# Optimization experiments

Hardware: AMD Instinct MI355X
Metric: run time of the kernel (lower is better)

## Reference

```python
import jax, jax.numpy as jnp
import numpy as np
import math

D_MODEL = 1024
N_HEADS = 16
D_HEAD = D_MODEL // N_HEADS
WINDOW = 256
SCALE = 1.0 / math.sqrt(D_HEAD)


def setup_inputs() -> dict:
    key = jax.random.key(0)
    kx, kqkv, kout = jax.random.split(key, 3)
    x = jax.random.normal(kx, (2, 2048, D_MODEL), dtype=jnp.float32)
    # xavier_uniform for nn.Linear weights (shape [out, in] in torch; store as [in, out] for x @ W)
    lim_qkv = math.sqrt(6.0 / (D_MODEL + 3 * D_MODEL))
    W_qkv = jax.random.uniform(kqkv, (D_MODEL, 3 * D_MODEL), dtype=jnp.float32, minval=-lim_qkv, maxval=lim_qkv)
    lim_out = math.sqrt(6.0 / (D_MODEL + D_MODEL))
    W_out = jax.random.uniform(kout, (D_MODEL, D_MODEL), dtype=jnp.float32, minval=-lim_out, maxval=lim_out)
    return {"x": x, "W_qkv": W_qkv, "W_out": W_out}


def _window_mask(seq_len: int) -> jnp.ndarray:
    # causal + sliding window: position i attends to j with i-WINDOW < j <= i
    i = jnp.arange(seq_len)[:, None]
    j = jnp.arange(seq_len)[None, :]
    allowed = (j <= i) & (j > i - WINDOW)
    return jnp.where(allowed, 0.0, -jnp.inf).astype(jnp.float32)


def reference(x, W_qkv, W_out):
    B, S, _ = x.shape
    qkv = x @ W_qkv                                   # [B, S, 3*D]
    qkv = qkv.reshape(B, S, 3, N_HEADS, D_HEAD)
    qkv = jnp.transpose(qkv, (2, 0, 3, 1, 4))         # [3, B, H, S, Dh]
    q, k, v = qkv[0], qkv[1], qkv[2]
    scores = jnp.einsum('bhsd,bhtd->bhst', q, k) * SCALE
    scores = scores + _window_mask(S)[None, None]
    weights = jax.nn.softmax(scores, axis=-1)
    out = jnp.einsum('bhst,bhtd->bhsd', weights, v)   # [B, H, S, Dh]
    out = jnp.transpose(out, (0, 2, 1, 3)).reshape(B, S, D_MODEL)
    return out @ W_out
```

## Files before the change

### kernel.cpp

```cpp
#include <hip/hip_runtime.h>

typedef unsigned short u16;
typedef unsigned int u32;

#define D_MODEL 1024
#define N_HEADS 16
#define D_HEAD 64
#define WIN 256
#define SEQ 2048
#define BATCH 2
#define NROWS (BATCH*SEQ)

typedef short frag_ab __attribute__((ext_vector_type(8)));
typedef float frag_cd __attribute__((ext_vector_type(4)));
typedef float f32x16 __attribute__((ext_vector_type(16)));
typedef u16 u16x8 __attribute__((ext_vector_type(8)));

__device__ __forceinline__ u16 f2bf(float f) {
    union { float f; u32 u; } x; x.f = f;
    u32 r = x.u + 0x7fffu + ((x.u >> 16) & 1u);
    return (u16)(r >> 16);
}

__device__ __forceinline__ void load_lds16(const void* g, void* l) {
    __builtin_amdgcn_global_load_lds(
        (const __attribute__((address_space(1))) void*)g,
        (__attribute__((address_space(3))) void*)l, 16, 0, 0);
}

__device__ __forceinline__ void transpose_tile(const float* __restrict__ W, u16* __restrict__ WT,
                                               int K, int N, int n0, int k0,
                                               int scale_rows, float scale, float (*tile)[33]) {
    int x = threadIdx.x & 31, y = threadIdx.x >> 5;
#pragma unroll
    for (int r = 0; r < 4; r++)
        tile[y + 8 * r][x] = W[(size_t)(k0 + y + 8 * r) * N + n0 + x];
    __syncthreads();
#pragma unroll
    for (int r = 0; r < 4; r++) {
        int nrow = n0 + y + 8 * r;
        float v = tile[x][y + 8 * r];
        if (nrow < scale_rows) v *= scale;
        WT[(size_t)nrow * K + k0 + x] = f2bf(v);
    }
}

__global__ __launch_bounds__(256) void prep_kernel(const float* __restrict__ x,
                                                   const float* __restrict__ W_qkv,
                                                   u16* __restrict__ xb,
                                                   u16* __restrict__ wqkvT,
                                                   float qscale) {
    __shared__ float tile[32][33];
    const int bid = blockIdx.x;
    if (bid < 4096) {
        int idx = bid * 256 + threadIdx.x;
        float4 v = ((const float4*)x)[idx];
        ushort4 o;
        o.x = f2bf(v.x); o.y = f2bf(v.y); o.z = f2bf(v.z); o.w = f2bf(v.w);
        ((ushort4*)xb)[idx] = o;
    } else {
        int t = bid - 4096;
        transpose_tile(W_qkv, wqkvT, D_MODEL, 3 * D_MODEL, (t % 96) * 32, (t / 96) * 32,
                       D_MODEL, qscale, tile);
    }
}

template <bool BF16_OUT, int BM, int MB, int NPER>
__global__ __launch_bounds__(256, 4) void gemm_bk64(const u16* __restrict__ A,
                                                    const u16* __restrict__ BT,
                                                    void* __restrict__ C,
                                                    int M, int N, int K) {
    constexpr int MT = BM / 64;
    __shared__ union SMem {
        struct { u16 As[BM * 64]; u16 Bs[128 * 64]; } s;
        u16 cs[BF16_OUT ? BM * 136 : 1];
    } sm;
    const int tid = threadIdx.x;
    const int xcd = blockIdx.x & 7, sblk = blockIdx.x >> 3;
    const int m0 = (sblk % MB) * BM;
    const int n0 = (xcd * NPER + sblk / MB) * 128;
    const int wave = tid >> 6, lane = tid & 63;
    const int wm = (wave >> 1) * (BM / 2), wn = (wave & 1) * 64;
    const int l32 = lane & 31, kh = lane >> 5;

    f32x16 acc[MT][2] = {};

    const int r0 = tid >> 3;
    const int w  = (tid & 7) ^ (r0 & 7);
    const u16* aP = A  + (size_t)(m0 + r0) * K + w * 8;
    const u16* bP = BT + (size_t)(n0 + r0) * K + w * 8;

    for (int k0 = 0; k0 < K; k0 += 64) {
        __syncthreads();
#pragma unroll
        for (int u = 0; u < BM / 32; u++)
            load_lds16(aP + (size_t)(32 * u) * K + k0, &sm.s.As[(tid + 256 * u) * 8]);
#pragma unroll
        for (int u = 0; u < 4; u++)
            load_lds16(bP + (size_t)(32 * u) * K + k0, &sm.s.Bs[(tid + 256 * u) * 8]);
        __syncthreads();

#pragma unroll
        for (int kk = 0; kk < 4; kk++) {
            const int csel = ((kk * 2 + kh) ^ (l32 & 7)) * 8;
            frag_ab af[MT], bf[2];
#pragma unroll
            for (int t = 0; t < MT; t++)
                af[t] = *(const frag_ab*)&sm.s.As[(wm + t * 32 + l32) * 64 + csel];
#pragma unroll
            for (int t = 0; t < 2; t++)
                bf[t] = *(const frag_ab*)&sm.s.Bs[(wn + t * 32 + l32) * 64 + csel];
#pragma unroll
            for (int mt = 0; mt < MT; mt++)
#pragma unroll
                for (int nt = 0; nt < 2; nt++)
                    acc[mt][nt] = __builtin_amdgcn_mfma_f32_32x32x16_bf16(af[mt], bf[nt], acc[mt][nt], 0, 0, 0);
        }
    }

    if constexpr (BF16_OUT) {
        __syncthreads();
#pragma unroll
        for (int mt = 0; mt < MT; mt++)
#pragma unroll
            for (int nt = 0; nt < 2; nt++) {
                int col = wn + nt * 32 + l32;
#pragma unroll
                for (int reg = 0; reg < 16; reg++) {
                    int row = wm + mt * 32 + (reg & 3) + 8 * (reg >> 2) + 4 * kh;
                    sm.cs[row * 136 + col] = f2bf(acc[mt][nt][reg]);
                }
            }
        __syncthreads();
        const int cc = tid & 15, rb = tid >> 4;
#pragma unroll
        for (int i = 0; i < BM / 16; i++) {
            int row = rb + 16 * i;
            u16x8 vv = *(const u16x8*)&sm.cs[row * 136 + cc * 8];
            *(u16x8*)((u16*)C + (size_t)(m0 + row) * N + n0 + cc * 8) = vv;
        }
    } else {
#pragma unroll
        for (int mt = 0; mt < MT; mt++)
#pragma unroll
            for (int nt = 0; nt < 2; nt++) {
                int col = n0 + wn + nt * 32 + l32;
#pragma unroll
                for (int reg = 0; reg < 16; reg++) {
                    int row = m0 + wm + mt * 32 + (reg & 3) + 8 * (reg >> 2) + 4 * kh;
                    ((float*)C)[(size_t)row * N + col] = acc[mt][nt][reg];
                }
            }
    }
}

__global__ __launch_bounds__(256) void attn_kernel(const u16* __restrict__ qkv, u16* __restrict__ out,
                                                   const float* __restrict__ W_out,
                                                   u16* __restrict__ woutT) {
    __shared__ u16 Ks[2][64 * 64];
    __shared__ u16 Vt[64 * 72];
    __shared__ u16 ps[4][16 * 72];

    if (blockIdx.x >= 1024) {
        int t = blockIdx.x - 1024;
        transpose_tile(W_out, woutT, D_MODEL, D_MODEL, (t & 31) * 32, (t >> 5) * 32,
                       0, 1.0f, (float(*)[33])&Ks[0][0]);
        return;
    }

    const int tid = threadIdx.x;
    const int wave = tid >> 6, lane = tid & 63;
    const int quad = lane >> 4, c16 = lane & 15;

    const int bh = blockIdx.x & 31;
    const int qc = blockIdx.x >> 5;
    const int h  = bh & 15;
    const int b  = bh >> 4;
    const int q0 = qc * 64;
    const int qw0 = q0 + wave * 16;

    frag_ab qf[2];
    {
        const u16* qrow = qkv + (size_t)(b * SEQ + qw0 + c16) * 3072 + h * 64;
        qf[0] = *(const frag_ab*)(qrow + quad * 8);
        qf[1] = *(const frag_ab*)(qrow + 32 + quad * 8);
    }

    float m_r[4], l_r[4];
    frag_cd acc[4] = {};

    const int ntiles = qc < 4 ? qc + 1 : 5;

    const int krow = wave * 16 + (lane >> 3);
    const int kchunk = (lane & 7) ^ (lane >> 3);
    const int vj2 = (tid & 31) * 2, vd8 = tid >> 5;

    const u16* kbase = qkv + (size_t)(b * SEQ + krow) * 3072 + 1024 + h * 64 + kchunk * 8;
    const u16* vbase = qkv + (size_t)(b * SEQ + vj2) * 3072 + 2048 + h * 64 + vd8 * 8;

    u16x8 va, vb;
    {
        const u16* g = kbase + (size_t)q0 * 3072;
        load_lds16(g,            &Ks[0][krow * 64 + (lane & 7) * 8]);
        load_lds16(g + 8 * 3072, &Ks[0][(krow + 8) * 64 + (lane & 7) * 8]);
        const u16* gv = vbase + (size_t)q0 * 3072;
        va = *(const u16x8*)gv;
        vb = *(const u16x8*)(gv + 3072);
#pragma unroll
        for (int dd = 0; dd < 8; dd++)
            *(u32*)&Vt[(vd8 * 8 + dd) * 72 + vj2] = (u32)va[dd] | ((u32)vb[dd] << 16);
    }

    for (int t = 0; t < ntiles; t++) {
        const int cur = t & 1, nxt = cur ^ 1;
        const int j0 = q0 - 64 * t;
        __syncthreads();
        const bool pre = (t + 1 < ntiles);
        if (pre) {
            const u16* g = kbase + (size_t)(j0 - 64) * 3072;
            load_lds16(g,            &Ks[nxt][krow * 64 + (lane & 7) * 8]);
            load_lds16(g + 8 * 3072, &Ks[nxt][(krow + 8) * 64 + (lane & 7) * 8]);
            const u16* gv = vbase + (size_t)(j0 - 64) * 3072;
            va = *(const u16x8*)gv;
            vb = *(const u16x8*)(gv + 3072);
        }

        frag_cd s[4] = {};
#pragma unroll
        for (int kb = 0; kb < 4; kb++) {
            frag_ab kf0 = *(const frag_ab*)&Ks[cur][(kb * 16 + c16) * 64 + ((quad    ) ^ (c16 & 7)) * 8];
            frag_ab kf1 = *(const frag_ab*)&Ks[cur][(kb * 16 + c16) * 64 + ((4 + quad) ^ (c16 & 7)) * 8];
            s[kb] = __builtin_amdgcn_mfma_f32_16x16x32_bf16(qf[0], kf0, s[kb], 0, 0, 0);
            s[kb] = __builtin_amdgcn_mfma_f32_16x16x32_bf16(qf[1], kf1, s[kb], 0, 0, 0);
        }

        if (t == 0) {
#pragma unroll
            for (int reg = 0; reg < 4; reg++) {
                const int i = qw0 + quad * 4 + reg;
#pragma unroll
                for (int kb = 0; kb < 4; kb++)
                    if (q0 + kb * 16 + c16 > i) s[kb][reg] = -1e30f;
            }
        } else if (t == 4) {
#pragma unroll
            for (int reg = 0; reg < 4; reg++) {
                const int i = qw0 + quad * 4 + reg;
#pragma unroll
                for (int kb = 0; kb < 4; kb++)
                    if (j0 + kb * 16 + c16 + WIN <= i) s[kb][reg] = -1e30f;
            }
        }

        float mt_[4];
#pragma unroll
        for (int reg = 0; reg < 4; reg++)
            mt_[reg] = fmaxf(fmaxf(s[0][reg], s[1][reg]), fmaxf(s[2][reg], s[3][reg]));
#pragma unroll
        for (int off = 1; off < 16; off <<= 1)
#pragma unroll
            for (int reg = 0; reg < 4; reg++) mt_[reg] = fmaxf(mt_[reg], __shfl_xor(mt_[reg], off));

        float alpha[4];
        if (t == 0) {
#pragma unroll
            for (int reg = 0; reg < 4; reg++) m_r[reg] = mt_[reg];
        } else {
#pragma unroll
            for (int reg = 0; reg < 4; reg++) {
                float mn = fmaxf(m_r[reg], mt_[reg]);
                alpha[reg] = __builtin_amdgcn_exp2f(m_r[reg] - mn);
                m_r[reg] = mn;
            }
        }

        float rs[4] = {0.f, 0.f, 0.f, 0.f};
#pragma unroll
        for (int kb = 0; kb < 4; kb++)
#pragma unroll
            for (int reg = 0; reg < 4; reg++) {
                float p = __builtin_amdgcn_exp2f(s[kb][reg] - m_r[reg]);
                union { float f; u32 u; } pu; pu.f = p;
                ps[wave][(quad * 4 + reg) * 72 + kb * 16 + c16] = (u16)(pu.u >> 16);
                rs[reg] += p;
            }
#pragma unroll
        for (int off = 1; off < 16; off <<= 1)
#pragma unroll
            for (int reg = 0; reg < 4; reg++) rs[reg] += __shfl_xor(rs[reg], off);

        if (t == 0) {
#pragma unroll
            for (int reg = 0; reg < 4; reg++) l_r[reg] = rs[reg];
        } else {
#pragma unroll
            for (int reg = 0; reg < 4; reg++) l_r[reg] = l_r[reg] * alpha[reg] + rs[reg];
#pragma unroll
            for (int dblk = 0; dblk < 4; dblk++)
#pragma unroll
                for (int reg = 0; reg < 4; reg++) acc[dblk][reg] *= alpha[reg];
        }

#pragma unroll
        for (int js = 0; js < 2; js++) {
            frag_ab pf = *(const frag_ab*)&ps[wave][c16 * 72 + js * 32 + quad * 8];
#pragma unroll
            for (int dblk = 0; dblk < 4; dblk++) {
                frag_ab vf = *(const frag_ab*)&Vt[(dblk * 16 + c16) * 72 + js * 32 + quad * 8];
                acc[dblk] = __builtin_amdgcn_mfma_f32_16x16x32_bf16(pf, vf, acc[dblk], 0, 0, 0);
            }
        }

        if (pre) {
            __syncthreads();
#pragma unroll
            for (int dd = 0; dd < 8; dd++)
                *(u32*)&Vt[(vd8 * 8 + dd) * 72 + vj2] = (u32)va[dd] | ((u32)vb[dd] << 16);
        }
    }

    float inv[4];
#pragma unroll
    for (int reg = 0; reg < 4; reg++) inv[reg] = 1.f / l_r[reg];
#pragma unroll
    for (int dblk = 0; dblk < 4; dblk++)
#pragma unroll
        for (int reg = 0; reg < 4; reg++)
            out[(size_t)(b * SEQ + qw0 + quad * 4 + reg) * 1024 + h * 64 + dblk * 16 + c16] =
                f2bf(acc[dblk][reg] * inv[reg]);
}

extern "C" void kernel_launch(void* const* d_in, const int* in_sizes, int n_in,
                              void* d_out, int out_size, void* d_ws, size_t ws_size,
                              hipStream_t stream) {
    const float* x     = (const float*)d_in[0];
    const float* W_qkv = (const float*)d_in[1];
    const float* W_out = (const float*)d_in[2];
    float* out = (float*)d_out;

    char* ws = (char*)d_ws;
    u16* xb    = (u16*)(ws);
    u16* wqkvT = (u16*)(ws + 8388608);
    u16* woutT = (u16*)(ws + 14680064);
    u16* qkvb  = (u16*)(ws + 16777216);
    u16* attnb = (u16*)(ws + 41943040);

    const float QSCALE = 0.125f * 1.4426950408889634f;

    prep_kernel<<<7168, 256, 0, stream>>>(x, W_qkv, xb, wqkvT, QSCALE);
    gemm_bk64<true, 128, 32, 3><<<768, 256, 0, stream>>>(
        xb, wqkvT, qkvb, NROWS, 3 * D_MODEL, D_MODEL);
    attn_kernel<<<2048, 256, 0, stream>>>(qkvb, attnb, W_out, woutT);
    gemm_bk64<false, 64, 64, 1><<<512, 256, 0, stream>>>(
        attnb, woutT, out, NROWS, D_MODEL, D_MODEL);
}
```

Measured before the change: 149.5 us.

## Add dedicated 256x192-tile double-buffered QKV GEMM kernel with 512 threads

```diff
diff --git a/kernel.cpp b/kernel.cpp
--- a/kernel.cpp
+++ b/kernel.cpp
@@ -65,6 +65,105 @@
     }
 }
 
+__global__ __launch_bounds__(512, 2) void gemm1_qkv(const u16* __restrict__ A,
+                                                    const u16* __restrict__ BT,
+                                                    u16* __restrict__ C) {
+    constexpr int K = 1024, NLD = 3072, NT = K >> 6;
+    __shared__ union SM {
+        struct { u16 As[2][256 * 64]; u16 Bs[2][192 * 64]; } s;
+        u16 cs[256 * 200];
+    } sm;
+    const int tid = threadIdx.x;
+    const int xcd = blockIdx.x & 7, sblk = blockIdx.x >> 3;
+    const int m0 = (sblk & 15) * 256;
+    const int n0 = (xcd * 2 + (sblk >> 4)) * 192;
+    const int wave = tid >> 6, lane = tid & 63;
+    const int wm = (wave >> 1) * 64, wn = (wave & 1) * 96;
+    const int l32 = lane & 31, kh = lane >> 5;
+
+    const int r0 = tid >> 3;
+    const int w  = (tid & 7) ^ (r0 & 7);
+    const u16* aP = A  + (size_t)(m0 + r0) * K + w * 8;
+    const u16* bP = BT + (size_t)(n0 + r0) * K + w * 8;
+
+    f32x16 acc[2][3] = {};
+
+#define STAGE(tile_, buf_) do {                                                   \
+        const int k0_ = (tile_) * 64;                                             \
+        _Pragma("unroll")                                                         \
+        for (int u = 0; u < 4; ++u)                                               \
+            load_lds16(aP + (size_t)(64 * u) * K + k0_,                           \
+                       &sm.s.As[buf_][(tid + 512 * u) * 8]);                      \
+        _Pragma("unroll")                                                         \
+        for (int u = 0; u < 3; ++u)                                               \
+            load_lds16(bP + (size_t)(64 * u) * K + k0_,                           \
+                       &sm.s.Bs[buf_][(tid + 512 * u) * 8]);                      \
+    } while (0)
+
+    STAGE(0, 0);
+    STAGE(1, 1);
+
+    int cur = 0;
+    for (int t = 0; t < NT; ++t) {
+        if (t + 1 < NT) asm volatile("s_waitcnt vmcnt(7)" ::: "memory");
+        else            asm volatile("s_waitcnt vmcnt(0)" ::: "memory");
+        asm volatile("s_barrier" ::: "memory");
+
+        const u16* As = sm.s.As[cur];
+        const u16* Bs = sm.s.Bs[cur];
+#pragma unroll
+        for (int ph = 0; ph < 2; ++ph) {
+            frag_ab af[2][2], bf[2][3];
+#pragma unroll
+            for (int kx = 0; kx < 2; ++kx) {
+                const int kk = ph * 2 + kx;
+                const int csel = ((kk * 2 + kh) ^ (l32 & 7)) * 8;
+#pragma unroll
+                for (int mt = 0; mt < 2; ++mt)
+                    af[kx][mt] = *(const frag_ab*)&As[(wm + mt * 32 + l32) * 64 + csel];
+#pragma unroll
+                for (int nt = 0; nt < 3; ++nt)
+                    bf[kx][nt] = *(const frag_ab*)&Bs[(wn + nt * 32 + l32) * 64 + csel];
+            }
+            asm volatile("s_barrier" ::: "memory");
+            __builtin_amdgcn_s_setprio(1);
+#pragma unroll
+            for (int kx = 0; kx < 2; ++kx)
+#pragma unroll
+                for (int mt = 0; mt < 2; ++mt)
+#pragma unroll
+                    for (int nt = 0; nt < 3; ++nt)
+                        acc[mt][nt] = __builtin_amdgcn_mfma_f32_32x32x16_bf16(
+                            af[kx][mt], bf[kx][nt], acc[mt][nt], 0, 0, 0);
+            __builtin_amdgcn_s_setprio(0);
+            asm volatile("s_barrier" ::: "memory");
+        }
+        if (t + 2 < NT) STAGE(t + 2, cur);
+        cur ^= 1;
+    }
+#undef STAGE
+
+#pragma unroll
+    for (int mt = 0; mt < 2; ++mt)
+#pragma unroll
+        for (int nt = 0; nt < 3; ++nt) {
+            const int col = wn + nt * 32 + l32;
+#pragma unroll
+            for (int reg = 0; reg < 16; ++reg) {
+                const int row = wm + mt * 32 + (reg & 3) + 8 * (reg >> 2) + 4 * kh;
+                sm.cs[row * 200 + col] = f2bf(acc[mt][nt][reg]);
+            }
+        }
+    asm volatile("s_barrier" ::: "memory");
+#pragma unroll
+    for (int i = 0; i < 12; ++i) {
+        const int idx = tid + 512 * i;
+        const int row = idx / 24, c8 = idx % 24;
+        u16x8 vv = *(const u16x8*)&sm.cs[row * 200 + c8 * 8];
+        *(u16x8*)(C + (size_t)(m0 + row) * NLD + n0 + c8 * 8) = vv;
+    }
+}
+
 template <bool BF16_OUT, int BM, int MB, int NPER>
 __global__ __launch_bounds__(256, 4) void gemm_bk64(const u16* __restrict__ A,
                                                     const u16* __restrict__ BT,
@@ -348,8 +447,7 @@
     const float QSCALE = 0.125f * 1.4426950408889634f;
 
     prep_kernel<<<7168, 256, 0, stream>>>(x, W_qkv, xb, wqkvT, QSCALE);
-    gemm_bk64<true, 128, 32, 3><<<768, 256, 0, stream>>>(
-        xb, wqkvT, qkvb, NROWS, 3 * D_MODEL, D_MODEL);
+    gemm1_qkv<<<256, 512, 0, stream>>>(xb, wqkvT, qkvb);
     attn_kernel<<<2048, 256, 0, stream>>>(qkvb, attnb, W_out, woutT);
     gemm_bk64<false, 64, 64, 1><<<512, 256, 0, stream>>>(
         attnb, woutT, out, NROWS, D_MODEL, D_MODEL);
```

Measured after the change: 151.6 us. About the same (+1.4%).

## Add specialized 128x96-tile QKV GEMM with 16x16x32 MFMA

Applied to the files above, without the earlier changes.

```diff
diff --git a/kernel.cpp b/kernel.cpp
--- a/kernel.cpp
+++ b/kernel.cpp
@@ -65,6 +65,80 @@
     }
 }
 
+__global__ __launch_bounds__(256, 4) void gemm1_96(const u16* __restrict__ A,
+                                                   const u16* __restrict__ BT,
+                                                   u16* __restrict__ C) {
+    constexpr int K = 1024, N = 3072;
+    __shared__ union SMem {
+        struct { u16 As[128 * 64]; u16 Bs[96 * 64]; } s;
+        u16 cs[128 * 104];
+    } sm;
+    const int tid = threadIdx.x;
+    const int xcd = blockIdx.x & 7, sblk = blockIdx.x >> 3;
+    const int m0 = (sblk & 31) * 128;
+    const int n0 = (xcd * 4 + (sblk >> 5)) * 96;
+    const int wave = tid >> 6, lane = tid & 63;
+    const int quad = lane >> 4, c16 = lane & 15;
+    const int wm = (wave >> 1) * 64, wn = (wave & 1) * 48;
+
+    const int r0 = tid >> 3;
+    const int w  = (tid & 7) ^ (r0 & 7);
+    const u16* aP = A  + (size_t)(m0 + r0) * K + w * 8;
+    const u16* bP = BT + (size_t)(n0 + r0) * K + w * 8;
+
+    frag_cd acc[4][3] = {};
+
+    for (int k0 = 0; k0 < K; k0 += 64) {
+        __syncthreads();
+#pragma unroll
+        for (int u = 0; u < 4; u++)
+            load_lds16(aP + (size_t)(32 * u) * K + k0, &sm.s.As[(tid + 256 * u) * 8]);
+#pragma unroll
+        for (int u = 0; u < 3; u++)
+            load_lds16(bP + (size_t)(32 * u) * K + k0, &sm.s.Bs[(tid + 256 * u) * 8]);
+        __syncthreads();
+
+#pragma unroll
+        for (int kk = 0; kk < 2; kk++) {
+            const int csel = ((kk * 4 + quad) ^ (c16 & 7)) * 8;
+            frag_ab af[4], bf[3];
+#pragma unroll
+            for (int fm = 0; fm < 4; fm++)
+                af[fm] = *(const frag_ab*)&sm.s.As[(wm + fm * 16 + c16) * 64 + csel];
+#pragma unroll
+            for (int fn = 0; fn < 3; fn++)
+                bf[fn] = *(const frag_ab*)&sm.s.Bs[(wn + fn * 16 + c16) * 64 + csel];
+#pragma unroll
+            for (int fm = 0; fm < 4; fm++)
+#pragma unroll
+                for (int fn = 0; fn < 3; fn++)
+                    acc[fm][fn] = __builtin_amdgcn_mfma_f32_16x16x32_bf16(
+                        af[fm], bf[fn], acc[fm][fn], 0, 0, 0);
+        }
+    }
+
+    __syncthreads();
+#pragma unroll
+    for (int fm = 0; fm < 4; fm++)
+#pragma unroll
+        for (int fn = 0; fn < 3; fn++) {
+            const int col = wn + fn * 16 + c16;
+#pragma unroll
+            for (int reg = 0; reg < 4; reg++) {
+                const int row = wm + fm * 16 + quad * 4 + reg;
+                sm.cs[row * 104 + col] = f2bf(acc[fm][fn][reg]);
+            }
+        }
+    __syncthreads();
+#pragma unroll
+    for (int i = 0; i < 6; i++) {
+        const int idx = tid + 256 * i;
+        const int row = idx / 12, c8 = idx % 12;
+        u16x8 vv = *(const u16x8*)&sm.cs[row * 104 + c8 * 8];
+        *(u16x8*)(C + (size_t)(m0 + row) * N + n0 + c8 * 8) = vv;
+    }
+}
+
 template <bool BF16_OUT, int BM, int MB, int NPER>
 __global__ __launch_bounds__(256, 4) void gemm_bk64(const u16* __restrict__ A,
                                                     const u16* __restrict__ BT,
@@ -348,8 +422,7 @@
     const float QSCALE = 0.125f * 1.4426950408889634f;
 
     prep_kernel<<<7168, 256, 0, stream>>>(x, W_qkv, xb, wqkvT, QSCALE);
-    gemm_bk64<true, 128, 32, 3><<<768, 256, 0, stream>>>(
-        xb, wqkvT, qkvb, NROWS, 3 * D_MODEL, D_MODEL);
+    gemm1_96<<<1024, 256, 0, stream>>>(xb, wqkvT, qkvb);
     attn_kernel<<<2048, 256, 0, stream>>>(qkvb, attnb, W_out, woutT);
     gemm_bk64<false, 64, 64, 1><<<512, 256, 0, stream>>>(
         attnb, woutT, out, NROWS, D_MODEL, D_MODEL);
```

Result: no change. 148.0 us (-1.0%).
